# Performance work log

Measured on AMD Instinct MI355X. Metric: run time of the kernel, lower is better.

## Reference

```python
import jax, jax.numpy as jnp
import numpy as np

B, T, D, H = 4, 4096, 1024, 16
DH = D // H
NB = T // 2 + 1  # rfft bins


def setup_inputs() -> dict:
    key = jax.random.key(0)
    ks = jax.random.split(key, 6)
    x = jax.random.normal(ks[0], (B, T, D), dtype=jnp.float32)
    # torch nn.Linear params: weight [out, in], bias [out]
    W_qkv = jax.random.normal(ks[1], (3 * D, D), dtype=jnp.float32) * 0.02
    b_qkv = jnp.zeros((3 * D,), dtype=jnp.float32)
    W_o = jax.random.normal(ks[2], (D, D), dtype=jnp.float32) * 0.02
    b_o = jnp.zeros((D,), dtype=jnp.float32)
    # per-head per-bin spectral filters (smart-init-like small values)
    log_gain = jax.random.normal(ks[3], (H, NB), dtype=jnp.float32) * 0.05
    phase = jax.random.normal(ks[4], (H, NB), dtype=jnp.float32) * 0.01
    return {"x": x, "W_qkv": W_qkv, "b_qkv": b_qkv, "W_o": W_o,
            "b_o": b_o, "log_gain": log_gain, "phase": phase}


def reference(x, W_qkv, b_qkv, W_o, b_o, log_gain, phase):
    # qkv projection; only v is used on the spectral path (q,k discarded)
    qkv = jnp.einsum('btd,ed->bte', x, W_qkv) + b_qkv  # [B,T,3D]
    v = qkv[..., 2 * D:]                               # [B,T,D]
    v = v.reshape(B, T, H, DH).transpose(0, 2, 1, 3)   # [B,H,T,DH]
    # rFFT along the token dim
    v_f = jnp.fft.rfft(v.astype(jnp.float32), axis=2)  # [B,H,NB,DH] complex
    # per-head per-bin complex filter: polar(exp(log_gain), phase)
    mag = jnp.exp(log_gain)
    comp = jax.lax.complex(mag * jnp.cos(phase), mag * jnp.sin(phase))  # [H,NB]
    v_f = v_f * comp[None, :, :, None]
    y_h = jnp.fft.irfft(v_f, n=T, axis=2)              # [B,H,T,DH]
    y = y_h.transpose(0, 2, 1, 3).reshape(B, T, D)     # [B,T,D]
    y = jnp.einsum('btd,ed->bte', y, W_o) + b_o
    return x + y
```

## Files before the change

kernel.cpp:

```cpp
#include <hip/hip_runtime.h>
#include <hip/hip_bf16.h>
#include <math.h>

#define B_BATCH 4
#define T_LEN   4096
#define D_DIM   1024
#define H_HEADS 16
#define NB_BINS 2049
#define M_ROWS  (B_BATCH * T_LEN)

typedef __attribute__((ext_vector_type(8))) short short8;
typedef __attribute__((ext_vector_type(8))) unsigned short u16x8;
typedef __attribute__((ext_vector_type(4))) float f32x4;

__device__ __forceinline__ ushort f2bf(float f) {
    unsigned b = __float_as_uint(f);
    unsigned r = (b + 0x7fffu + ((b >> 16) & 1u)) >> 16;
    return (ushort)r;
}
__device__ __forceinline__ float bf2f(ushort u) {
    return __uint_as_float(((unsigned)u) << 16);
}

__global__ void cvt_f32_to_bf16(const float* __restrict__ src, ushort* __restrict__ dst, int n4) {
    int i = blockIdx.x * 256 + threadIdx.x;
    if (i >= n4) return;
    float4 v = ((const float4*)src)[i];
    ushort4 o;
    o.x = f2bf(v.x); o.y = f2bf(v.y); o.z = f2bf(v.z); o.w = f2bf(v.w);
    ((ushort4*)dst)[i] = o;
}

__global__ void cvt_weights(const float* __restrict__ wv, const float* __restrict__ wo,
                            ushort* __restrict__ wvb, ushort* __restrict__ wob, int n4) {
    int i = blockIdx.x * 256 + threadIdx.x;
    const float* src = (i < n4) ? wv : wo;
    ushort* dst = (i < n4) ? wvb : wob;
    int j = (i < n4) ? i : (i - n4);
    float4 v = ((const float4*)src)[j];
    ushort4 o;
    o.x = f2bf(v.x); o.y = f2bf(v.y); o.z = f2bf(v.z); o.w = f2bf(v.w);
    ((ushort4*)dst)[j] = o;
}

__device__ __forceinline__ int drev16(int i) {
    return ((i & 15) << 8) | (i & 0xF0) | (i >> 8);
}

__global__ void prep_tables(const float* __restrict__ lg, const float* __restrict__ ph,
                            float2* __restrict__ Cdr, float2* __restrict__ tw) {
    int idx = blockIdx.x * 256 + threadIdx.x;
    if (idx < 4096) {
        double th = -2.0 * 3.14159265358979323846 * (double)idx / 4096.0;
        tw[idx] = make_float2((float)cos(th), (float)sin(th));
    }
    if (idx >= H_HEADS * 4096) return;
    int h = idx >> 12, i = idx & 4095;
    int f = drev16(i);
    int fc = (f <= 2048) ? f : (4096 - f);
    float sgn = (f <= 2048) ? 1.f : -1.f;
    float m = expf(lg[h * NB_BINS + fc]) * (1.0f / 4096.0f);
    float p = ph[h * NB_BINS + fc];
    float re = m * __cosf(p), im = sgn * m * __sinf(p);
    if (fc == 0 || fc == 2048) im = 0.f;
    Cdr[idx] = make_float2(re, im);
}

template<bool RESID, bool BIASROW>
__global__ __launch_bounds__(256) void gemm128(const ushort* __restrict__ A,
        const ushort* __restrict__ Bm, const float* __restrict__ bias,
        const float* __restrict__ resid, void* __restrict__ Cout,
        int M, int N, int K) {
    __shared__ ushort lds[24576];
    const int tid  = threadIdx.x;
    const int lane = tid & 63;
    const int wid  = tid >> 6;
    const int wr   = wid >> 1, wc = wid & 1;
    const int fr   = lane & 15;
    const int nbn  = N >> 7;
    int bid = (int)blockIdx.x;
    bid = (bid & 7) * ((int)gridDim.x >> 3) + (bid >> 3);
    const int bm = bid / nbn, bn = bid % nbn;
    const int row0 = bm << 7, col0 = bn << 7;
    const int NT = K >> 5;

    f32x4 acc[4][4];
#pragma unroll
    for (int i = 0; i < 4; i++)
#pragma unroll
        for (int j = 0; j < 4; j++) acc[i][j] = (f32x4){0.f, 0.f, 0.f, 0.f};

    auto stage = [&](const ushort* P, int gr0, int k0, int lb) {
#pragma unroll
        for (int i = 0; i < 2; i++) {
            int r = (wid << 5) + (i << 4) + (lane >> 2);
            int c = ((lane & 3) ^ ((lane >> 3) & 3)) << 3;
            const ushort* g = P + (size_t)(gr0 + r) * (size_t)K + (size_t)(k0 + c);
            __builtin_amdgcn_global_load_lds(
                (const __attribute__((address_space(1))) void*)g,
                (__attribute__((address_space(3))) void*)&lds[lb + (((wid << 1) + i) << 9)],
                16, 0, 0);
        }
    };
    auto rdfrag = [&](int base, int row) -> short8 {
        int g = (((lane >> 4) ^ ((row >> 1) & 3)) << 3);
        return *(const short8*)&lds[base + (row << 5) + g];
    };

    stage(A,  row0, 0, 0);    stage(Bm, col0, 0, 12288);
    stage(A,  row0, 32, 4096); stage(Bm, col0, 32, 12288 + 4096);
    asm volatile("s_waitcnt vmcnt(4)" ::: "memory");
    __builtin_amdgcn_sched_barrier(0);
    __builtin_amdgcn_s_barrier();

    short8 aF[4], bF[4];
    for (int t = 0; t < NT; ++t) {
        const int cb = (t % 3) << 12;
        const int sb = ((t + 2) % 3) << 12;
        const bool st = (t + 2) < NT;
        const int k2 = (t + 2) << 5;

#pragma unroll
        for (int mi = 0; mi < 4; mi++) aF[mi] = rdfrag(cb, (wr << 6) + (mi << 4) + fr);
#pragma unroll
        for (int ni = 0; ni < 4; ni++) bF[ni] = rdfrag(12288 + cb, (wc << 6) + (ni << 4) + fr);
        if (st) { stage(A, row0, k2, sb); stage(Bm, col0, k2, 12288 + sb); }
        __builtin_amdgcn_s_barrier();
        asm volatile("s_waitcnt lgkmcnt(0)" ::: "memory");
        __builtin_amdgcn_sched_barrier(0);
        __builtin_amdgcn_s_setprio(1);
#pragma unroll
        for (int mi = 0; mi < 4; mi++)
#pragma unroll
            for (int ni = 0; ni < 4; ni++)
                acc[mi][ni] = __builtin_amdgcn_mfma_f32_16x16x32_bf16(aF[mi], bF[ni], acc[mi][ni], 0, 0, 0);
        __builtin_amdgcn_s_setprio(0);
        __builtin_amdgcn_sched_barrier(0);
        if (t + 1 < NT) {
            if (st) asm volatile("s_waitcnt vmcnt(4)" ::: "memory");
            else    asm volatile("s_waitcnt vmcnt(0)" ::: "memory");
        }
        __builtin_amdgcn_s_barrier();
    }

    const int crow = (lane >> 4) << 2;
#pragma unroll
    for (int mi = 0; mi < 4; mi++) {
#pragma unroll
        for (int ni = 0; ni < 4; ni++) {
            int row = row0 + (wr << 6) + (mi << 4) + crow;
            int col = col0 + (wc << 6) + (ni << 4) + fr;
            float bcol = BIASROW ? 0.f : bias[col];
#pragma unroll
            for (int j = 0; j < 4; j++) {
                float v = acc[mi][ni][j] + (BIASROW ? bias[row + j] : bcol);
                size_t off = (size_t)(row + j) * N + col;
                if (RESID) ((float*)Cout)[off] = resid[off] + v;
                else       ((ushort*)Cout)[off] = f2bf(v);
            }
        }
    }
}

__device__ __forceinline__ float2 cadd(float2 a, float2 b){ return make_float2(a.x+b.x, a.y+b.y); }
__device__ __forceinline__ float2 csub(float2 a, float2 b){ return make_float2(a.x-b.x, a.y-b.y); }
__device__ __forceinline__ float2 jmulp(float2 z){ return make_float2(-z.y, z.x); }
__device__ __forceinline__ float2 cmul(float2 a, float2 b){
    return make_float2(fmaf(a.x,b.x,-a.y*b.y), fmaf(a.x,b.y, a.y*b.x)); }
__device__ __forceinline__ float2 cmulc(float2 a, float2 b){
    return make_float2(fmaf(a.x,b.x, a.y*b.y), fmaf(a.y,b.x,-a.x*b.y)); }

template<int INV>
__device__ __forceinline__ void bf4(float2& a, float2& b, float2& c, float2& d) {
    float2 acp = cadd(a,c), acm = csub(a,c);
    float2 bdp = cadd(b,d), bdm = csub(b,d);
    float2 jb  = jmulp(bdm);
    a = cadd(acp, bdp);
    c = csub(acp, bdp);
    if (INV) { b = cadd(acm, jb); d = csub(acm, jb); }
    else     { b = csub(acm, jb); d = cadd(acm, jb); }
}

#define C16_1 0.9238795325112867f
#define S16_1 0.3826834323650898f
#define R16_2 0.7071067811865476f

template<int INV>
__device__ __forceinline__ void dft16(float2 v[16]) {
    const float sg = INV ? 1.f : -1.f;
    bf4<INV>(v[0], v[4], v[8],  v[12]);
    bf4<INV>(v[1], v[5], v[9],  v[13]);
    bf4<INV>(v[2], v[6], v[10], v[14]);
    bf4<INV>(v[3], v[7], v[11], v[15]);
    const float2 w1 = make_float2( C16_1, sg*S16_1);
    const float2 w2 = make_float2( R16_2, sg*R16_2);
    const float2 w3 = make_float2( S16_1, sg*C16_1);
    const float2 w6 = make_float2(-R16_2, sg*R16_2);
    const float2 w9 = make_float2(-C16_1,-sg*S16_1);
    v[5]  = cmul(v[5],  w1);
    v[6]  = cmul(v[6],  w2);
    v[7]  = cmul(v[7],  w3);
    v[9]  = cmul(v[9],  w2);
    v[10] = INV ? jmulp(v[10]) : make_float2(v[10].y, -v[10].x);
    v[11] = cmul(v[11], w6);
    v[13] = cmul(v[13], w3);
    v[14] = cmul(v[14], w6);
    v[15] = cmul(v[15], w9);
    bf4<INV>(v[0],  v[1],  v[2],  v[3]);
    bf4<INV>(v[4],  v[5],  v[6],  v[7]);
    bf4<INV>(v[8],  v[9],  v[10], v[11]);
    bf4<INV>(v[12], v[13], v[14], v[15]);
}

__host__ __device__ constexpr int oidx(int r) { return ((r & 3) << 2) | (r >> 2); }

template<int INV>
__device__ __forceinline__ void dft16p(float2 v[16]) {
    const float sg = INV ? 1.f : -1.f;
    bf4<INV>(v[oidx(0)], v[oidx(4)], v[oidx(8)],  v[oidx(12)]);
    bf4<INV>(v[oidx(1)], v[oidx(5)], v[oidx(9)],  v[oidx(13)]);
    bf4<INV>(v[oidx(2)], v[oidx(6)], v[oidx(10)], v[oidx(14)]);
    bf4<INV>(v[oidx(3)], v[oidx(7)], v[oidx(11)], v[oidx(15)]);
    const float2 w1 = make_float2( C16_1, sg*S16_1);
    const float2 w2 = make_float2( R16_2, sg*R16_2);
    const float2 w3 = make_float2( S16_1, sg*C16_1);
    const float2 w6 = make_float2(-R16_2, sg*R16_2);
    const float2 w9 = make_float2(-C16_1,-sg*S16_1);
    v[oidx(5)]  = cmul(v[oidx(5)],  w1);
    v[oidx(6)]  = cmul(v[oidx(6)],  w2);
    v[oidx(7)]  = cmul(v[oidx(7)],  w3);
    v[oidx(9)]  = cmul(v[oidx(9)],  w2);
    v[oidx(10)] = INV ? jmulp(v[oidx(10)]) : make_float2(v[oidx(10)].y, -v[oidx(10)].x);
    v[oidx(11)] = cmul(v[oidx(11)], w6);
    v[oidx(13)] = cmul(v[oidx(13)], w3);
    v[oidx(14)] = cmul(v[oidx(14)], w6);
    v[oidx(15)] = cmul(v[oidx(15)], w9);
    bf4<INV>(v[oidx(0)],  v[oidx(1)],  v[oidx(2)],  v[oidx(3)]);
    bf4<INV>(v[oidx(4)],  v[oidx(5)],  v[oidx(6)],  v[oidx(7)]);
    bf4<INV>(v[oidx(8)],  v[oidx(9)],  v[oidx(10)], v[oidx(11)]);
    bf4<INV>(v[oidx(12)], v[oidx(13)], v[oidx(14)], v[oidx(15)]);
}

__device__ __forceinline__ int phz(int t) { return t ^ (((t >> 4) ^ (t >> 8)) & 15); }

template<typename F>
__device__ __forceinline__ void tw_powers(float2 w1, F&& apply) {
    apply(1, w1);
    float2 w2 = cmul(w1, w1);   apply(2, w2);
    float2 w3 = cmul(w2, w1);   apply(3, w3);
    float2 w4 = cmul(w2, w2);   apply(4, w4);
    float2 w5 = cmul(w4, w1);   apply(5, w5);
    float2 w6 = cmul(w4, w2);   apply(6, w6);
    float2 w7 = cmul(w4, w3);   apply(7, w7);
    float2 w8 = cmul(w4, w4);   apply(8, w8);
    apply(9,  cmul(w8, w1));
    apply(10, cmul(w8, w2));
    apply(11, cmul(w8, w3));
    apply(12, cmul(w8, w4));
    apply(13, cmul(w8, w5));
    apply(14, cmul(w8, w6));
    apply(15, cmul(w8, w7));
}

__global__ __launch_bounds__(256) void fft16_filter(const ushort* __restrict__ VT,
                                                    ushort* __restrict__ yT,
                                                    const float2* __restrict__ tw,
                                                    const float2* __restrict__ Cdr) {
    __shared__ float2 X[2][4096];
    const int tid = threadIdx.x;
    const int b   = blockIdx.x >> 8;
    const int qb  = blockIdx.x & 255;
    const int d0  = qb << 2;
    const int h   = qb >> 4;

    float2 v[2][16];
#pragma unroll
    for (int p = 0; p < 2; p++) {
        const ushort* sRe = VT + (size_t)(d0 + 2 * p) * M_ROWS + b * T_LEN;
        const ushort* sIm = VT + (size_t)(d0 + 2 * p + 1) * M_ROWS + b * T_LEN;
#pragma unroll
        for (int j = 0; j < 16; j++)
            v[p][j] = make_float2(bf2f(sRe[tid + (j << 8)]), bf2f(sIm[tid + (j << 8)]));
    }

    dft16<0>(v[0]);
    dft16<0>(v[1]);
    {
        float2 w1 = tw[tid];
        tw_powers(w1, [&](int r, float2 w) {
            v[0][oidx(r)] = cmul(v[0][oidx(r)], w);
            v[1][oidx(r)] = cmul(v[1][oidx(r)], w);
        });
    }
#pragma unroll
    for (int r = 0; r < 16; r++) {
        int a = phz(tid + (r << 8));
        X[0][a] = v[0][oidx(r)];
        X[1][a] = v[1][oidx(r)];
    }
    __syncthreads();

    const int p2 = tid & 15, g2 = tid >> 4;
    const int base2 = (g2 << 8) + p2;
#pragma unroll
    for (int j = 0; j < 16; j++) {
        int a = phz(base2 + (j << 4));
        v[0][j] = X[0][a];
        v[1][j] = X[1][a];
    }
    dft16<0>(v[0]);
    dft16<0>(v[1]);
#pragma unroll
    for (int r = 1; r < 16; r++) {
        float2 w = tw[(p2 * r) << 4];
        v[0][oidx(r)] = cmul(v[0][oidx(r)], w);
        v[1][oidx(r)] = cmul(v[1][oidx(r)], w);
    }
#pragma unroll
    for (int r = 0; r < 16; r++) {
        int a = phz(base2 + (r << 4));
        X[0][a] = v[0][oidx(r)];
        X[1][a] = v[1][oidx(r)];
    }
    __syncthreads();

    const int base3 = tid << 4;
#pragma unroll
    for (int j = 0; j < 16; j++) {
        int a = phz(base3 + j);
        v[0][j] = X[0][a];
        v[1][j] = X[1][a];
    }
    dft16<0>(v[0]);
    dft16<0>(v[1]);
    const float2* Ch = Cdr + (h << 12) + base3;
#pragma unroll
    for (int r = 0; r < 16; r++) {
        float2 c = Ch[r];
        v[0][oidx(r)] = cmul(v[0][oidx(r)], c);
        v[1][oidx(r)] = cmul(v[1][oidx(r)], c);
    }
    dft16p<1>(v[0]);
    dft16p<1>(v[1]);
#pragma unroll
    for (int r = 0; r < 16; r++) {
        int a = phz(base3 + r);
        X[0][a] = v[0][r];
        X[1][a] = v[1][r];
    }
    __syncthreads();

#pragma unroll
    for (int j = 0; j < 16; j++) {
        int a = phz(base2 + (j << 4));
        v[0][j] = X[0][a];
        v[1][j] = X[1][a];
    }
#pragma unroll
    for (int j = 1; j < 16; j++) {
        float2 w = tw[(p2 * j) << 4];
        v[0][j] = cmulc(v[0][j], w);
        v[1][j] = cmulc(v[1][j], w);
    }
    dft16<1>(v[0]);
    dft16<1>(v[1]);
#pragma unroll
    for (int r = 0; r < 16; r++) {
        int a = phz(base2 + (r << 4));
        X[0][a] = v[0][oidx(r)];
        X[1][a] = v[1][oidx(r)];
    }
    __syncthreads();

#pragma unroll
    for (int j = 0; j < 16; j++) {
        int a = phz(tid + (j << 8));
        v[0][j] = X[0][a];
        v[1][j] = X[1][a];
    }
    {
        float2 w1 = tw[tid];
        tw_powers(w1, [&](int r, float2 w) {
            v[0][r] = cmulc(v[0][r], w);
            v[1][r] = cmulc(v[1][r], w);
        });
    }
    dft16<1>(v[0]);
    dft16<1>(v[1]);
#pragma unroll
    for (int p = 0; p < 2; p++) {
        ushort* dRe = yT + (size_t)(d0 + 2 * p) * M_ROWS + b * T_LEN;
        ushort* dIm = yT + (size_t)(d0 + 2 * p + 1) * M_ROWS + b * T_LEN;
#pragma unroll
        for (int r = 0; r < 16; r++) {
            float2 val = v[p][oidx(r)];
            dRe[tid + (r << 8)] = f2bf(val.x);
            dIm[tid + (r << 8)] = f2bf(val.y);
        }
    }
}

__global__ __launch_bounds__(256) void transpose_yT(const ushort* __restrict__ src,
                                                    ushort* __restrict__ dst) {
    __shared__ ushort tile[4096];
    const int tid = threadIdx.x;
    const int bm = blockIdx.x & 255;
    const int bd = blockIdx.x >> 8;
    const int m0 = bm << 6, d0 = bd << 6;
#pragma unroll
    for (int i = 0; i < 2; i++) {
        int vn = tid + (i << 8);
        int r  = vn >> 3;
        int c8 = (vn & 7) << 3;
        u16x8 val = *(const u16x8*)&src[(size_t)(d0 + r) * M_ROWS + m0 + c8];
#pragma unroll
        for (int q = 0; q < 8; q++)
            tile[(r << 6) | ((c8 + q) ^ r)] = (ushort)val[q];
    }
    __syncthreads();
    const int dc = tid & 63;
    const int wb = tid >> 6;
#pragma unroll
    for (int i = 0; i < 16; i++) {
        int mr = wb + (i << 2);
        dst[(size_t)(m0 + mr) * D_DIM + d0 + dc] = tile[(dc << 6) | (mr ^ dc)];
    }
}

extern "C" void kernel_launch(void* const* d_in, const int* in_sizes, int n_in,
                              void* d_out, int out_size, void* d_ws, size_t ws_size,
                              hipStream_t stream) {
    const float* x    = (const float*)d_in[0];
    const float* Wqkv = (const float*)d_in[1];
    const float* bqkv = (const float*)d_in[2];
    const float* Wo   = (const float*)d_in[3];
    const float* bo   = (const float*)d_in[4];
    const float* lg   = (const float*)d_in[5];
    const float* ph   = (const float*)d_in[6];

    char* ws = (char*)d_ws;
    ushort* xb  = (ushort*)ws;
    ushort* Wvb = (ushort*)(ws + 33554432);
    ushort* Wob = (ushort*)(ws + 35651584);
    float2* tw  = (float2*)(ws + 37748736);
    float2* Cdr = (float2*)(ws + 37781504);

    ushort* VT   = (ushort*)d_out;
    ushort* yT   = (ushort*)((char*)d_out + 33554432);
    ushort* ynat = xb;
    float*  out  = (float*)d_out;

    prep_tables<<<(H_HEADS * 4096) / 256, 256, 0, stream>>>(lg, ph, Cdr, tw);
    cvt_f32_to_bf16<<<(16777216 / 4) / 256, 256, 0, stream>>>(x, xb, 16777216 / 4);
    cvt_weights<<<2 * (1048576 / 4) / 256, 256, 0, stream>>>(
        Wqkv + 2048 * 1024, Wo, Wvb, Wob, 1048576 / 4);

    gemm128<false, true><<<(D_DIM / 128) * (M_ROWS / 128), 256, 0, stream>>>(
        Wvb, xb, bqkv + 2 * D_DIM, nullptr, (void*)VT, D_DIM, M_ROWS, D_DIM);

    fft16_filter<<<B_BATCH * (D_DIM / 4), 256, 0, stream>>>(VT, yT, tw, Cdr);

    transpose_yT<<<(M_ROWS / 64) * (D_DIM / 64), 256, 0, stream>>>(yT, ynat);

    gemm128<true, false><<<(M_ROWS / 128) * (D_DIM / 128), 256, 0, stream>>>(
        ynat, Wob, bo, x, (void*)out, M_ROWS, D_DIM, D_DIM);
}
```

Before: 176.7 us.

## Fuse x bf16 conversion into V-projection GEMM and shrink tiles to 64x128

Removes the standalone fp32-to-bf16 conversion of x. The first GEMM now loads fp32 x tiles through registers, packs them to bf16 and writes them to LDS inside the main loop. Both GEMMs switch from 128x128 tiles with a 3-stage async pipeline to 64x128 tiles with double buffering, plain __syncthreads and a higher occupancy hint, which doubles the number of blocks. This saves a full pass over x, but the fp32 B path reads twice the bytes through registers and the smaller tiles lower data reuse per block.

```diff
diff --git a/kernel.cpp b/kernel.cpp
--- a/kernel.cpp
+++ b/kernel.cpp
@@ -21,14 +21,11 @@
 __device__ __forceinline__ float bf2f(ushort u) {
     return __uint_as_float(((unsigned)u) << 16);
 }
-
-__global__ void cvt_f32_to_bf16(const float* __restrict__ src, ushort* __restrict__ dst, int n4) {
-    int i = blockIdx.x * 256 + threadIdx.x;
-    if (i >= n4) return;
-    float4 v = ((const float4*)src)[i];
-    ushort4 o;
-    o.x = f2bf(v.x); o.y = f2bf(v.y); o.z = f2bf(v.z); o.w = f2bf(v.w);
-    ((ushort4*)dst)[i] = o;
+__device__ __forceinline__ u16x8 pack8(const float4& a, const float4& b) {
+    u16x8 o;
+    o[0] = f2bf(a.x); o[1] = f2bf(a.y); o[2] = f2bf(a.z); o[3] = f2bf(a.w);
+    o[4] = f2bf(b.x); o[5] = f2bf(b.y); o[6] = f2bf(b.z); o[7] = f2bf(b.w);
+    return o;
 }
 
 __global__ void cvt_weights(const float* __restrict__ wv, const float* __restrict__ wo,
@@ -66,12 +63,12 @@
     Cdr[idx] = make_float2(re, im);
 }
 
-template<bool RESID, bool BIASROW>
-__global__ __launch_bounds__(256) void gemm128(const ushort* __restrict__ A,
-        const ushort* __restrict__ Bm, const float* __restrict__ bias,
+template<bool RESID, bool BIASROW, bool BF32>
+__global__ __launch_bounds__(256, 4) void gemm64(const ushort* __restrict__ A,
+        const void* __restrict__ Bv, const float* __restrict__ bias,
         const float* __restrict__ resid, void* __restrict__ Cout,
         int M, int N, int K) {
-    __shared__ ushort lds[24576];
+    __shared__ ushort lds[12288];
     const int tid  = threadIdx.x;
     const int lane = tid & 63;
     const int wid  = tid >> 6;
@@ -81,25 +78,57 @@
     int bid = (int)blockIdx.x;
     bid = (bid & 7) * ((int)gridDim.x >> 3) + (bid >> 3);
     const int bm = bid / nbn, bn = bid % nbn;
-    const int row0 = bm << 7, col0 = bn << 7;
+    const int row0 = bm << 6, col0 = bn << 7;
     const int NT = K >> 5;
 
-    f32x4 acc[4][4];
-#pragma unroll
-    for (int i = 0; i < 4; i++)
+    const ushort* Bu = (const ushort*)Bv;
+    const float*  Bf = (const float*)Bv;
+
+    f32x4 acc[2][4];
+#pragma unroll
+    for (int i = 0; i < 2; i++)
 #pragma unroll
         for (int j = 0; j < 4; j++) acc[i][j] = (f32x4){0.f, 0.f, 0.f, 0.f};
 
-    auto stage = [&](const ushort* P, int gr0, int k0, int lb) {
+    auto stageA = [&](int t) {
+        int base = (t & 1) * 6144;
+        int row = tid >> 2;
+        int cs = (tid & 3) ^ ((tid >> 3) & 3);
+        const ushort* g = A + (size_t)(row0 + row) * (size_t)K + (size_t)((t << 5) + (cs << 3));
+        __builtin_amdgcn_global_load_lds(
+            (const __attribute__((address_space(1))) void*)g,
+            (__attribute__((address_space(3))) void*)&lds[base + (wid << 9)],
+            16, 0, 0);
+    };
+    auto stageB = [&](int t) {
+        int base = (t & 1) * 6144 + 2048;
 #pragma unroll
         for (int i = 0; i < 2; i++) {
-            int r = (wid << 5) + (i << 4) + (lane >> 2);
-            int c = ((lane & 3) ^ ((lane >> 3) & 3)) << 3;
-            const ushort* g = P + (size_t)(gr0 + r) * (size_t)K + (size_t)(k0 + c);
+            int s = (i << 8) + tid;
+            int row = s >> 2;
+            int cs = (s & 3) ^ ((s >> 3) & 3);
+            const ushort* g = Bu + (size_t)(col0 + row) * (size_t)K + (size_t)((t << 5) + (cs << 3));
             __builtin_amdgcn_global_load_lds(
                 (const __attribute__((address_space(1))) void*)g,
-                (__attribute__((address_space(3))) void*)&lds[lb + (((wid << 1) + i) << 9)],
+                (__attribute__((address_space(3))) void*)&lds[base + (i << 11) + (wid << 9)],
                 16, 0, 0);
+        }
+    };
+    auto issueB = [&](int t, float4 bR[4]) {
+        int row = tid >> 1;
+        const float* g = Bf + (size_t)(col0 + row) * (size_t)K
+                       + (size_t)((t << 5) + ((tid & 1) << 4));
+        bR[0] = *(const float4*)g;       bR[1] = *(const float4*)(g + 4);
+        bR[2] = *(const float4*)(g + 8); bR[3] = *(const float4*)(g + 12);
+    };
+    auto writeB = [&](int t, float4 bR[4]) {
+        int base = (t & 1) * 6144 + 2048;
+        int row = tid >> 1;
+        int cn0 = (tid & 1) << 1;
+#pragma unroll
+        for (int j = 0; j < 2; j++) {
+            int pos = (cn0 + j) ^ ((row >> 1) & 3);
+            *(u16x8*)&lds[base + (row << 5) + (pos << 3)] = pack8(bR[2 * j], bR[2 * j + 1]);
         }
     };
     auto rdfrag = [&](int base, int row) -> short8 {
@@ -107,48 +136,41 @@
         return *(const short8*)&lds[base + (row << 5) + g];
     };
 
-    stage(A,  row0, 0, 0);    stage(Bm, col0, 0, 12288);
-    stage(A,  row0, 32, 4096); stage(Bm, col0, 32, 12288 + 4096);
-    asm volatile("s_waitcnt vmcnt(4)" ::: "memory");
-    __builtin_amdgcn_sched_barrier(0);
-    __builtin_amdgcn_s_barrier();
-
-    short8 aF[4], bF[4];
+    stageA(0);
+    if (BF32) { float4 bR[4]; issueB(0, bR); writeB(0, bR); }
+    else      stageB(0);
+    __syncthreads();
+
     for (int t = 0; t < NT; ++t) {
-        const int cb = (t % 3) << 12;
-        const int sb = ((t + 2) % 3) << 12;
-        const bool st = (t + 2) < NT;
-        const int k2 = (t + 2) << 5;
-
-#pragma unroll
-        for (int mi = 0; mi < 4; mi++) aF[mi] = rdfrag(cb, (wr << 6) + (mi << 4) + fr);
-#pragma unroll
-        for (int ni = 0; ni < 4; ni++) bF[ni] = rdfrag(12288 + cb, (wc << 6) + (ni << 4) + fr);
-        if (st) { stage(A, row0, k2, sb); stage(Bm, col0, k2, 12288 + sb); }
-        __builtin_amdgcn_s_barrier();
-        asm volatile("s_waitcnt lgkmcnt(0)" ::: "memory");
-        __builtin_amdgcn_sched_barrier(0);
-        __builtin_amdgcn_s_setprio(1);
-#pragma unroll
-        for (int mi = 0; mi < 4; mi++)
+        const bool pre = (t + 1) < NT;
+        float4 bR[4];
+        if (pre) {
+            stageA(t + 1);
+            if (BF32) issueB(t + 1, bR);
+            else      stageB(t + 1);
+        }
+        const int ab = (t & 1) * 6144;
+        const int bb = ab + 2048;
+        short8 aF[2], bF[4];
+#pragma unroll
+        for (int ni = 0; ni < 4; ni++) bF[ni] = rdfrag(bb, (wc << 6) + (ni << 4) + fr);
+#pragma unroll
+        for (int mi = 0; mi < 2; mi++) aF[mi] = rdfrag(ab, (wr << 5) + (mi << 4) + fr);
+#pragma unroll
+        for (int mi = 0; mi < 2; mi++)
 #pragma unroll
             for (int ni = 0; ni < 4; ni++)
                 acc[mi][ni] = __builtin_amdgcn_mfma_f32_16x16x32_bf16(aF[mi], bF[ni], acc[mi][ni], 0, 0, 0);
-        __builtin_amdgcn_s_setprio(0);
-        __builtin_amdgcn_sched_barrier(0);
-        if (t + 1 < NT) {
-            if (st) asm volatile("s_waitcnt vmcnt(4)" ::: "memory");
-            else    asm volatile("s_waitcnt vmcnt(0)" ::: "memory");
-        }
-        __builtin_amdgcn_s_barrier();
+        if (BF32 && pre) writeB(t + 1, bR);
+        __syncthreads();
     }
 
     const int crow = (lane >> 4) << 2;
 #pragma unroll
-    for (int mi = 0; mi < 4; mi++) {
+    for (int mi = 0; mi < 2; mi++) {
 #pragma unroll
         for (int ni = 0; ni < 4; ni++) {
-            int row = row0 + (wr << 6) + (mi << 4) + crow;
+            int row = row0 + (wr << 5) + (mi << 4) + crow;
             int col = col0 + (wc << 6) + (ni << 4) + fr;
             float bcol = BIASROW ? 0.f : bias[col];
 #pragma unroll
@@ -439,7 +461,7 @@
     const float* ph   = (const float*)d_in[6];
 
     char* ws = (char*)d_ws;
-    ushort* xb  = (ushort*)ws;
+    ushort* ynat = (ushort*)ws;
     ushort* Wvb = (ushort*)(ws + 33554432);
     ushort* Wob = (ushort*)(ws + 35651584);
     float2* tw  = (float2*)(ws + 37748736);
@@ -447,21 +469,19 @@
 
     ushort* VT   = (ushort*)d_out;
     ushort* yT   = (ushort*)((char*)d_out + 33554432);
-    ushort* ynat = xb;
     float*  out  = (float*)d_out;
 
     prep_tables<<<(H_HEADS * 4096) / 256, 256, 0, stream>>>(lg, ph, Cdr, tw);
-    cvt_f32_to_bf16<<<(16777216 / 4) / 256, 256, 0, stream>>>(x, xb, 16777216 / 4);
     cvt_weights<<<2 * (1048576 / 4) / 256, 256, 0, stream>>>(
         Wqkv + 2048 * 1024, Wo, Wvb, Wob, 1048576 / 4);
 
-    gemm128<false, true><<<(D_DIM / 128) * (M_ROWS / 128), 256, 0, stream>>>(
-        Wvb, xb, bqkv + 2 * D_DIM, nullptr, (void*)VT, D_DIM, M_ROWS, D_DIM);
+    gemm64<false, true, true><<<(D_DIM / 64) * (M_ROWS / 128), 256, 0, stream>>>(
+        Wvb, (const void*)x, bqkv + 2 * D_DIM, nullptr, (void*)VT, D_DIM, M_ROWS, D_DIM);
 
     fft16_filter<<<B_BATCH * (D_DIM / 4), 256, 0, stream>>>(VT, yT, tw, Cdr);
 
     transpose_yT<<<(M_ROWS / 64) * (D_DIM / 64), 256, 0, stream>>>(yT, ynat);
 
-    gemm128<true, false><<<(M_ROWS / 128) * (D_DIM / 128), 256, 0, stream>>>(
-        ynat, Wob, bo, x, (void*)out, M_ROWS, D_DIM, D_DIM);
-}
+    gemm64<true, false, false><<<(M_ROWS / 64) * (D_DIM / 128), 256, 0, stream>>>(
+        ynat, (const void*)Wob, bo, x, (void*)out, M_ROWS, D_DIM, D_DIM);
+}
```

Result: slower. 271.1 us (+53.4%).
